# Kernel optimization log

Hardware: AMD Instinct MI355X
Metric: run time of the kernel (lower is better)

## Reference

```python
import jax, jax.numpy as jnp
import numpy as np

B, L, DM, H, DH = 2, 2048, 1024, 4, 128
TOT = H * DH  # 512


def _dwconv(x, w, b, L):
    # x: (B,L,C), w: (C,1,4) depthwise, padding=3 then causal trim to L (matches Conv1d(padding=3)[...,:L])
    y = jax.lax.conv_general_dilated(x.transpose(0, 2, 1), w, (1,), [(3, 3)],
                                     dimension_numbers=('NCH', 'OIH', 'NCH'),
                                     feature_group_count=w.shape[0])
    y = y[..., :L] + b[None, :, None]
    return y.transpose(0, 2, 1)


def _l2norm(x):
    return x / jnp.maximum(jnp.linalg.norm(x, axis=-1, keepdims=True), 1e-12)


def setup_inputs() -> dict:
    key = jax.random.key(0)
    ks = jax.random.split(key, 16)
    s = 0.02
    return {
        'x': jax.random.normal(ks[0], (B, L, DM), jnp.float32),
        'state': jnp.zeros((B, H, DH, DH), jnp.float32),
        'Wq': jax.random.normal(ks[1], (TOT, DM), jnp.float32) * s,
        'Wk': jax.random.normal(ks[2], (TOT, DM), jnp.float32) * s,
        'Wv': jax.random.normal(ks[3], (2 * TOT, DM), jnp.float32) * s,
        'Wa': jax.random.normal(ks[4], (H, DM), jnp.float32) * s,
        'Wb': jax.random.normal(ks[5], (H, DM), jnp.float32) * s,
        'Wg': jax.random.normal(ks[6], (TOT, DM), jnp.float32) * s,
        'Wo': jax.random.normal(ks[7], (DM, TOT), jnp.float32) * s,
        'qcw': jax.random.normal(ks[8], (TOT, 1, 4), jnp.float32) * 0.1,
        'qcb': jnp.zeros((TOT,), jnp.float32),
        'kcw': jax.random.normal(ks[9], (TOT, 1, 4), jnp.float32) * 0.1,
        'kcb': jnp.zeros((TOT,), jnp.float32),
        'vcw': jax.random.normal(ks[10], (2 * TOT, 1, 4), jnp.float32) * 0.1,
        'vcb': jnp.zeros((2 * TOT,), jnp.float32),
        'ln_w': jnp.ones((TOT,), jnp.float32),
        'ln_b': jnp.zeros((TOT,), jnp.float32),
    }


def reference(x, state, Wq, Wk, Wv, Wa, Wb, Wg, Wo, qcw, qcb, kcw, kcb, vcw, vcb, ln_w, ln_b):
    Bn, Ln, _ = x.shape
    q = _dwconv(x @ Wq.T, qcw, qcb, Ln)
    k = _dwconv(x @ Wk.T, kcw, kcb, Ln)
    v = _dwconv(x @ Wv.T, vcw, vcb, Ln)
    # silu then L2-normalize over the FULL total_dim (before head split), as in the source
    q = _l2norm(jax.nn.silu(q))
    k = _l2norm(jax.nn.silu(k))
    v = jax.nn.silu(v)
    alpha = jax.nn.sigmoid(x @ Wa.T)  # (B,L,H)
    beta = jax.nn.sigmoid(x @ Wb.T)   # (B,L,H)
    q = q.reshape(Bn, Ln, H, DH)
    k = k.reshape(Bn, Ln, H, DH)
    v_main, v_gate = jnp.split(v, 2, axis=-1)
    v_main = v_main.reshape(Bn, Ln, H, DH)
    v_gate = v_gate.reshape(Bn, Ln, H, DH)

    def step(S, inp):
        q_t, k_t, v_t, a_t, b_t = inp  # (B,H,D),(B,H,D),(B,H,D),(B,H),(B,H)
        a = a_t[..., None, None]
        b = b_t[..., None, None]
        Sk = jnp.einsum('bhij,bhj->bhi', S, k_t)  # S @ k
        # S @ (alpha*(I - beta k k^T)) + beta v k^T, via rank-1 update
        S = a * (S - b * (Sk[..., :, None] * k_t[..., None, :])) \
            + b * (v_t[..., :, None] * k_t[..., None, :])
        o = jnp.einsum('bhij,bhj->bhi', S, q_t)
        return S, o

    xs = (q.transpose(1, 0, 2, 3), k.transpose(1, 0, 2, 3), v_main.transpose(1, 0, 2, 3),
          alpha.transpose(1, 0, 2), beta.transpose(1, 0, 2))
    final_state, outs = jax.lax.scan(step, state, xs)
    out = outs.transpose(1, 0, 2, 3)  # (B,L,H,D)

    out = (out * v_gate).reshape(Bn, Ln, TOT)
    out = out * jax.nn.silu(x @ Wg.T)
    mu = out.mean(-1, keepdims=True)
    var = jnp.mean((out - mu) ** 2, axis=-1, keepdims=True)
    out = (out - mu) * jax.lax.rsqrt(var + 1e-5) * ln_w + ln_b
    out = out @ Wo.T
    return out, final_state
```

## Files before the change

kernel.cpp:

```cpp
#include <hip/hip_runtime.h>
#include <hip/hip_bf16.h>

#define BQ    2
#define LQ    2048
#define DMQ   1024
#define HQ    4
#define DHQ   128
#define TOTQ  512
#define BLQ   4096
#define NPROJ 2688
#define KPROJ 1024
#define CT    64
#define NCH   32

typedef short bf16x8 __attribute__((ext_vector_type(8)));
typedef short s16x4  __attribute__((ext_vector_type(4)));
typedef float f32x4  __attribute__((ext_vector_type(4)));

#define MFMA16(a, b, c) __builtin_amdgcn_mfma_f32_16x16x32_bf16(a, b, c, 0, 0, 0)

__device__ __forceinline__ float siluf(float x) { return x / (1.f + __expf(-x)); }
__device__ __forceinline__ float sigf(float x)  { return 1.f / (1.f + __expf(-x)); }
__device__ __forceinline__ short bf16s(float x) {
  return __builtin_bit_cast(short, __float2bfloat16(x));
}
__device__ __forceinline__ float bfu2f(unsigned short u) {
  return __bfloat162float(__builtin_bit_cast(__hip_bfloat16, u));
}
__device__ __forceinline__ bf16x8 pack8(f32x4 a, f32x4 b) {
  bf16x8 r;
  r[0] = bf16s(a.x); r[1] = bf16s(a.y); r[2] = bf16s(a.z); r[3] = bf16s(a.w);
  r[4] = bf16s(b.x); r[5] = bf16s(b.y); r[6] = bf16s(b.z); r[7] = bf16s(b.w);
  return r;
}

__device__ __forceinline__ void gload_lds16(const void* g, void* l) {
  __builtin_amdgcn_global_load_lds(
      (__attribute__((address_space(1))) void*)(unsigned long long)g,
      (__attribute__((address_space(3))) void*)(unsigned int)(unsigned long long)l,
      16, 0, 0);
}

__global__ __launch_bounds__(256)
void cast_f32_bf16_kernel(const float* __restrict__ src, __hip_bfloat16* __restrict__ dst, int n4)
{
  int i = blockIdx.x * 256 + threadIdx.x;
  if (i < n4) {
    float4 v = ((const float4*)src)[i];
    __hip_bfloat16 o[4] = { __float2bfloat16(v.x), __float2bfloat16(v.y),
                            __float2bfloat16(v.z), __float2bfloat16(v.w) };
    *(ushort4*)((unsigned short*)dst + (size_t)i * 4) = *(ushort4*)o;
  }
}

__global__ __launch_bounds__(256)
void cast_wcat_kernel(const float* __restrict__ Wq, const float* __restrict__ Wk,
                      const float* __restrict__ Wv, const float* __restrict__ Wg,
                      const float* __restrict__ Wa, const float* __restrict__ Wb,
                      __hip_bfloat16* __restrict__ Wcat)
{
  int i4 = blockIdx.x * 256 + threadIdx.x;
  int row = i4 >> 8;
  int col = (i4 & 255) * 4;
  int idx = row * 1024 + col;
  float4 v;
  if      (row < 512)  v = *(const float4*)(Wq + idx);
  else if (row < 1024) v = *(const float4*)(Wk + idx - 512 * 1024);
  else if (row < 2048) v = *(const float4*)(Wv + idx - 1024 * 1024);
  else if (row < 2560) v = *(const float4*)(Wg + idx - 2048 * 1024);
  else if (row < 2564) v = *(const float4*)(Wa + (row - 2560) * 1024 + col);
  else if (row < 2568) v = *(const float4*)(Wb + (row - 2564) * 1024 + col);
  else                 v = make_float4(0.f, 0.f, 0.f, 0.f);
  __hip_bfloat16 o[4] = { __float2bfloat16(v.x), __float2bfloat16(v.y),
                          __float2bfloat16(v.z), __float2bfloat16(v.w) };
  *(ushort4*)((unsigned short*)Wcat + idx) = *(ushort4*)o;
}

template <typename TOUT>
__global__ __launch_bounds__(256)
void gemm_bt_kernel(const __hip_bfloat16* __restrict__ A,
                    const __hip_bfloat16* __restrict__ Bw,
                    TOUT* __restrict__ C, int M, int N, int K,
                    float* __restrict__ aux, int auxc0)
{
  __shared__ __hip_bfloat16 As[2 * 128 * 32];
  __shared__ __hip_bfloat16 Bs[2 * 128 * 32];
  const int tid  = threadIdx.x;
  const int lane = tid & 63;
  const int w    = tid >> 6;
  const int wm   = w >> 1, wn = w & 1;
  const int tm   = blockIdx.x, tn = blockIdx.y;
  const int lr   = lane & 15, lk = lane >> 4;

  f32x4 acc[4][4] = {};

  const int e0   = tid * 8;
  const int srow = e0 >> 5;
  const int scol = e0 & 31;
  const __hip_bfloat16* Ap = A  + (size_t)(tm * 128 + srow) * K + scol;
  const __hip_bfloat16* Bp = Bw + (size_t)(tn * 128 + srow) * K + scol;
  char* AsB  = (char*)As;
  char* BsB  = (char*)Bs;
  const size_t half = (size_t)64 * K;
  const int nk = K >> 5;

  {
    char* AsD = AsB + w * 1024;
    char* BsD = BsB + w * 1024;
    gload_lds16(Ap,        AsD);
    gload_lds16(Ap + half, AsD + 4096);
    gload_lds16(Bp,        BsD);
    gload_lds16(Bp + half, BsD + 4096);
  }
  __syncthreads();

  for (int it = 0; it < nk; ++it) {
    const int sel = it & 1;
    if (it + 1 < nk) {
      const int kk = (it + 1) * 32;
      char* AsD = AsB + ((sel ^ 1) * 8192) + w * 1024;
      char* BsD = BsB + ((sel ^ 1) * 8192) + w * 1024;
      gload_lds16(Ap + kk,        AsD);
      gload_lds16(Ap + half + kk, AsD + 4096);
      gload_lds16(Bp + kk,        BsD);
      gload_lds16(Bp + half + kk, BsD + 4096);
    }
    const char* AsR = AsB + sel * 8192;
    const char* BsR = BsB + sel * 8192;
    bf16x8 af[4], bfv[4];
#pragma unroll
    for (int m = 0; m < 4; ++m)
      af[m]  = *(const bf16x8*)(AsR + ((wm * 64 + m * 16 + lr) * 32 + lk * 8) * 2);
#pragma unroll
    for (int n = 0; n < 4; ++n)
      bfv[n] = *(const bf16x8*)(BsR + ((wn * 64 + n * 16 + lr) * 32 + lk * 8) * 2);
#pragma unroll
    for (int m = 0; m < 4; ++m)
#pragma unroll
      for (int n = 0; n < 4; ++n)
        acc[m][n] = MFMA16(af[m], bfv[n], acc[m][n]);
    __syncthreads();
  }

  const int crow0 = tm * 128 + wm * 64 + (lane >> 4) * 4;
  const int ccol0 = tn * 128 + wn * 64 + lr;
#pragma unroll
  for (int m = 0; m < 4; ++m)
#pragma unroll
    for (int n = 0; n < 4; ++n) {
      const int cc = ccol0 + n * 16;
#pragma unroll
      for (int j = 0; j < 4; ++j) {
        const float v = acc[m][n][j];
        const size_t row = (size_t)(crow0 + m * 16 + j);
        if constexpr (sizeof(TOUT) == 2)
          ((unsigned short*)C)[row * N + cc] = (unsigned short)bf16s(v);
        else
          C[row * N + cc] = v;
        if (aux && cc >= auxc0 && cc < auxc0 + 8)
          aux[row * 8 + (cc - auxc0)] = v;
      }
    }
}

__global__ __launch_bounds__(256)
void conv_act_kernel(const __hip_bfloat16* __restrict__ C, const float* __restrict__ abf,
                     const float* __restrict__ qcw, const float* __restrict__ qcb,
                     const float* __restrict__ kcw, const float* __restrict__ kcb,
                     const float* __restrict__ vcw, const float* __restrict__ vcb,
                     __hip_bfloat16* __restrict__ qh, __hip_bfloat16* __restrict__ kh,
                     __hip_bfloat16* __restrict__ vm, __hip_bfloat16* __restrict__ vg,
                     float* __restrict__ al, float* __restrict__ be)
{
  const int blk = blockIdx.x;
  const int bl0 = blk * 8;
  const int t0  = bl0 & (LQ - 1);
  const int tid = threadIdx.x;
  const unsigned short* Cu = (const unsigned short*)C;
  __shared__ float red[4][16];

  float2 qv[8], kv[8];
  float sq[8], sk[8];
#pragma unroll
  for (int t = 0; t < 8; ++t) { sq[t] = 0.f; sk[t] = 0.f; }

  {
    const int c0 = tid * 2;
    const float4 wqA = *(const float4*)(qcw + 4 * c0);
    const float4 wqB = *(const float4*)(qcw + 4 * c0 + 4);
    const float4 wkA = *(const float4*)(kcw + 4 * c0);
    const float4 wkB = *(const float4*)(kcw + 4 * c0 + 4);
    const float2 bq = *(const float2*)(qcb + c0);
    const float2 bk = *(const float2*)(kcb + c0);
    float2 wrq[11], wrk[11];
#pragma unroll
    for (int r = 0; r < 11; ++r) {
      const int tt = t0 - 3 + r;
      if (tt >= 0) {
        const unsigned short* Cr = Cu + (size_t)(bl0 - 3 + r) * NPROJ;
        const ushort2 aq = *(const ushort2*)(Cr + c0);
        const ushort2 ak = *(const ushort2*)(Cr + 512 + c0);
        wrq[r] = make_float2(bfu2f(aq.x), bfu2f(aq.y));
        wrk[r] = make_float2(bfu2f(ak.x), bfu2f(ak.y));
      } else {
        wrq[r] = make_float2(0.f, 0.f);
        wrk[r] = make_float2(0.f, 0.f);
      }
    }
#pragma unroll
    for (int t = 0; t < 8; ++t) {
      float aq0 = bq.x, aq1 = bq.y, ak0 = bk.x, ak1 = bk.y;
#pragma unroll
      for (int j = 0; j < 4; ++j) {
        aq0 = fmaf(((const float*)&wqA)[j], wrq[t + j].x, aq0);
        aq1 = fmaf(((const float*)&wqB)[j], wrq[t + j].y, aq1);
        ak0 = fmaf(((const float*)&wkA)[j], wrk[t + j].x, ak0);
        ak1 = fmaf(((const float*)&wkB)[j], wrk[t + j].y, ak1);
      }
      const float q0 = siluf(aq0), q1 = siluf(aq1);
      const float k0 = siluf(ak0), k1 = siluf(ak1);
      qv[t] = make_float2(q0, q1);
      kv[t] = make_float2(k0, k1);
      sq[t] = fmaf(q1, q1, fmaf(q0, q0, sq[t]));
      sk[t] = fmaf(k1, k1, fmaf(k0, k0, sk[t]));
    }
  }
#pragma unroll
  for (int m = 1; m < 64; m <<= 1) {
#pragma unroll
    for (int t = 0; t < 8; ++t) {
      sq[t] += __shfl_xor(sq[t], m);
      sk[t] += __shfl_xor(sk[t], m);
    }
  }
  {
    const int w = tid >> 6, lane = tid & 63;
    if (lane == 0) {
#pragma unroll
      for (int t = 0; t < 8; ++t) { red[w][t] = sq[t]; red[w][8 + t] = sk[t]; }
    }
  }
  __syncthreads();
  float rnq[8], rnk[8];
#pragma unroll
  for (int t = 0; t < 8; ++t) {
    const float SQ = red[0][t] + red[1][t] + red[2][t] + red[3][t];
    const float SK = red[0][8 + t] + red[1][8 + t] + red[2][8 + t] + red[3][8 + t];
    rnq[t] = 1.f / fmaxf(sqrtf(SQ), 1e-12f);
    rnk[t] = 1.f / fmaxf(sqrtf(SK), 1e-12f);
  }
  {
    const int c0 = tid * 2;
#pragma unroll
    for (int t = 0; t < 8; ++t) {
      ushort2 oq, ok;
      oq.x = (unsigned short)bf16s(qv[t].x * rnq[t]);
      oq.y = (unsigned short)bf16s(qv[t].y * rnq[t]);
      ok.x = (unsigned short)bf16s(kv[t].x * rnk[t]);
      ok.y = (unsigned short)bf16s(kv[t].y * rnk[t]);
      *(ushort2*)((unsigned short*)qh + (size_t)(bl0 + t) * 512 + c0) = oq;
      *(ushort2*)((unsigned short*)kh + (size_t)(bl0 + t) * 512 + c0) = ok;
    }
  }
  {
    const int cv = tid * 4;
    const float4 wv0 = *(const float4*)(vcw + 4 * cv);
    const float4 wv1 = *(const float4*)(vcw + 4 * cv + 4);
    const float4 wv2 = *(const float4*)(vcw + 4 * cv + 8);
    const float4 wv3 = *(const float4*)(vcw + 4 * cv + 12);
    const float4 bv4 = *(const float4*)(vcb + cv);
    float4 wr[11];
#pragma unroll
    for (int r = 0; r < 11; ++r) {
      const int tt = t0 - 3 + r;
      if (tt >= 0) {
        const ushort4 u = *(const ushort4*)(Cu + (size_t)(bl0 - 3 + r) * NPROJ + 1024 + cv);
        wr[r] = make_float4(bfu2f(u.x), bfu2f(u.y), bfu2f(u.z), bfu2f(u.w));
      } else {
        wr[r] = make_float4(0.f, 0.f, 0.f, 0.f);
      }
    }
#pragma unroll
    for (int t = 0; t < 8; ++t) {
      float a0 = bv4.x, a1 = bv4.y, a2 = bv4.z, a3 = bv4.w;
#pragma unroll
      for (int j = 0; j < 4; ++j) {
        a0 = fmaf(((const float*)&wv0)[j], ((const float*)&wr[t + j])[0], a0);
        a1 = fmaf(((const float*)&wv1)[j], ((const float*)&wr[t + j])[1], a1);
        a2 = fmaf(((const float*)&wv2)[j], ((const float*)&wr[t + j])[2], a2);
        a3 = fmaf(((const float*)&wv3)[j], ((const float*)&wr[t + j])[3], a3);
      }
      ushort4 o;
      o.x = (unsigned short)bf16s(siluf(a0));
      o.y = (unsigned short)bf16s(siluf(a1));
      o.z = (unsigned short)bf16s(siluf(a2));
      o.w = (unsigned short)bf16s(siluf(a3));
      if (cv < 512) *(ushort4*)((unsigned short*)vm + (size_t)(bl0 + t) * 512 + cv)         = o;
      else          *(ushort4*)((unsigned short*)vg + (size_t)(bl0 + t) * 512 + (cv - 512)) = o;
    }
  }
  if (tid < 64) {
    const int t = tid >> 3;
    const int k = tid & 7;
    const float v = abf[(size_t)(bl0 + t) * 8 + k];
    if (k < 4) al[(size_t)(bl0 + t) * 4 + k]       = sigf(v);
    else       be[(size_t)(bl0 + t) * 4 + (k - 4)] = sigf(v);
  }
}

__global__ __launch_bounds__(256)
void scan_phaseA_kernel(const __hip_bfloat16* __restrict__ qh, const __hip_bfloat16* __restrict__ kh,
                        const __hip_bfloat16* __restrict__ vm, const float* __restrict__ al,
                        const float* __restrict__ be,
                        short* __restrict__ WTB, short* __restrict__ ZB,
                        short* __restrict__ PHB, float* __restrict__ GV,
                        short* __restrict__ TRB, float* __restrict__ BF)
{
  __shared__ char sm[136192];
  float* Xl = (float*)(sm);
  __hip_bfloat16* KBl = (__hip_bfloat16*)(sm);
  __hip_bfloat16* QBl = (__hip_bfloat16*)(sm + 17408);
  float* Ll  = (float*)(sm + 65536);
  float* dv  = (float*)(sm + 82944);
  float* bv  = (float*)(sm + 83200);
  float* gbv = (float*)(sm + 83456);
  float* fvs = (float*)(sm + 83712);
  short* KTl  = (short*)(sm + 83968);
  short* WTFl = (short*)(sm + 101376);
  short* ZFl  = (short*)(sm + 118784);

  const int cb = blockIdx.x;
  const int bh = cb & 7, c = cb >> 3;
  const int b = bh >> 2, h = bh & 3;
  const int tid = threadIdx.x;
  const int lane = tid & 63;
  const int w = tid >> 6;
  const int lr = lane & 15, lk = lane >> 4;
  const size_t rowbase = (size_t)(b * LQ + c * CT) * 512 + h * 128;

#pragma unroll
  for (int rep = 0; rep < 4; ++rep) {
    const int fid = tid + rep * 256;
    const int r = fid >> 4;
    const int cg = (fid & 15) * 8;
    *(bf16x8*)(KBl + r * 136 + cg) = *(const bf16x8*)(kh + rowbase + (size_t)r * 512 + cg);
    *(bf16x8*)(QBl + r * 136 + cg) = *(const bf16x8*)(qh + rowbase + (size_t)r * 512 + cg);
  }
  if (w == 0) {
    float la = __logf(al[(size_t)(b * LQ + c * CT + lane) * 4 + h]);
    const float bb = be[(size_t)(b * LQ + c * CT + lane) * 4 + h];
#pragma unroll
    for (int off = 1; off < 64; off <<= 1) {
      const float tv = __shfl_up(la, off, 64);
      if (lane >= off) la += tv;
    }
    dv[lane] = la; bv[lane] = bb; gbv[lane] = bb * __expf(la);
    const float d63 = __shfl(la, 63, 64);
    fvs[lane] = __expf(d63 - la);
    GV[cb * 64 + lane] = __expf(la);
  }
  __syncthreads();

  f32x4 aG[4] = {}, aP[4] = {};
#pragma unroll
  for (int ks = 0; ks < 4; ++ks) {
    bf16x8 bk[4];
#pragma unroll
    for (int nt = 0; nt < 4; ++nt)
      bk[nt] = *(const bf16x8*)(KBl + (nt * 16 + lr) * 136 + ks * 32 + lk * 8);
    const bf16x8 ak = *(const bf16x8*)(KBl + (w * 16 + lr) * 136 + ks * 32 + lk * 8);
    const bf16x8 aq = *(const bf16x8*)(QBl + (w * 16 + lr) * 136 + ks * 32 + lk * 8);
#pragma unroll
    for (int nt = 0; nt < 4; ++nt) {
      aG[nt] = MFMA16(ak, bk[nt], aG[nt]);
      aP[nt] = MFMA16(aq, bk[nt], aP[nt]);
    }
  }
#pragma unroll
  for (int nt = 0; nt < 4; ++nt)
#pragma unroll
    for (int jj = 0; jj < 4; ++jj) {
      const int t = w * 16 + lk * 4 + jj;
      const int s = nt * 16 + lr;
      const float eg = __expf(dv[t] - dv[s]);
      Ll[t * 68 + s] = (t > s) ? bv[t] * eg * aG[nt][jj] : 0.f;
      PHB[(size_t)cb * 4096 + t * 64 + s] = (s <= t) ? bf16s(eg * aP[nt][jj]) : (short)0;
    }
  if (tid < 128) {
    const short* Kbs = (const short*)KBl;
#pragma unroll
    for (int s4 = 0; s4 < 16; ++s4) {
      s16x4 pk;
#pragma unroll
      for (int e = 0; e < 4; ++e)
        pk[e] = Kbs[(s4 * 4 + e) * 136 + tid];
      *(s16x4*)(KTl + tid * 68 + s4 * 4) = pk;
    }
  }
  __syncthreads();

  const int j = tid;
  const __hip_bfloat16* src = (j < 128) ? kh : vm;
  const __hip_bfloat16* xp = src + rowbase + (j & 127);
  float* XlC = Xl + j;
  short* dstN = (j < 128) ? (WTB + (size_t)cb * 8192 + j)
                          : (ZB  + (size_t)cb * 8192 + (j - 128));
  short* dstT = (j < 128) ? (WTFl + j * 68)
                          : (ZFl  + (j - 128) * 68);

  for (int r = 0; r < 4; ++r) {
    float u[16];
#pragma unroll
    for (int i = 0; i < 16; ++i) {
      const int t = r * 16 + i;
      u[i] = __bfloat162float(xp[(size_t)t * 512]) * ((j < 128) ? gbv[t] : bv[t]);
    }
    for (int sc = 0; sc < r; ++sc) {
      float xs[16];
#pragma unroll
      for (int k = 0; k < 16; ++k) xs[k] = XlC[(sc * 16 + k) * 256];
#pragma unroll
      for (int i = 0; i < 16; ++i) {
        const float* lrow = Ll + (r * 16 + i) * 68 + sc * 16;
        const f32x4 l0 = *(const f32x4*)(lrow);
        const f32x4 l1 = *(const f32x4*)(lrow + 4);
        const f32x4 l2 = *(const f32x4*)(lrow + 8);
        const f32x4 l3 = *(const f32x4*)(lrow + 12);
        f32x4 acc = {};
        acc.x = fmaf(l0.x, xs[0],  acc.x); acc.y = fmaf(l0.y, xs[1],  acc.y);
        acc.z = fmaf(l0.z, xs[2],  acc.z); acc.w = fmaf(l0.w, xs[3],  acc.w);
        acc.x = fmaf(l1.x, xs[4],  acc.x); acc.y = fmaf(l1.y, xs[5],  acc.y);
        acc.z = fmaf(l1.z, xs[6],  acc.z); acc.w = fmaf(l1.w, xs[7],  acc.w);
        acc.x = fmaf(l2.x, xs[8],  acc.x); acc.y = fmaf(l2.y, xs[9],  acc.y);
        acc.z = fmaf(l2.z, xs[10], acc.z); acc.w = fmaf(l2.w, xs[11], acc.w);
        acc.x = fmaf(l3.x, xs[12], acc.x); acc.y = fmaf(l3.y, xs[13], acc.y);
        acc.z = fmaf(l3.z, xs[14], acc.z); acc.w = fmaf(l3.w, xs[15], acc.w);
        u[i] -= (acc.x + acc.y) + (acc.z + acc.w);
      }
    }
#pragma unroll
    for (int i = 1; i < 16; ++i) {
      const float* lrow = Ll + (r * 16 + i) * 68 + r * 16;
      f32x4 acc = {};
#pragma unroll
      for (int k4 = 0; k4 < 4; ++k4) {
        if (k4 * 4 < i) {
          const f32x4 lv = *(const f32x4*)(lrow + k4 * 4);
          acc.x = fmaf(lv.x, u[k4 * 4 + 0], acc.x);
          acc.y = fmaf(lv.y, u[k4 * 4 + 1], acc.y);
          acc.z = fmaf(lv.z, u[k4 * 4 + 2], acc.z);
          acc.w = fmaf(lv.w, u[k4 * 4 + 3], acc.w);
        }
      }
      u[i] -= (acc.x + acc.y) + (acc.z + acc.w);
    }
    if (r < 3) {
#pragma unroll
      for (int i = 0; i < 16; ++i) XlC[(r * 16 + i) * 256] = u[i];
    }
#pragma unroll
    for (int i = 0; i < 16; ++i)
      dstN[(r * 16 + i) * 128] = bf16s(u[i]);
#pragma unroll
    for (int s4 = 0; s4 < 4; ++s4) {
      s16x4 p;
#pragma unroll
      for (int e = 0; e < 4; ++e)
        p[e] = bf16s(fvs[r * 16 + s4 * 4 + e] * u[s4 * 4 + e]);
      *(s16x4*)(dstT + r * 16 + s4 * 4) = p;
    }
  }
  __syncthreads();

  const float gc = __expf(dv[63]);
  {
    f32x4 acc[2][8] = {};
#pragma unroll
    for (int ks = 0; ks < 2; ++ks) {
      const bf16x8 a0 = *(const bf16x8*)(KTl + (w * 32 + lr) * 68 + ks * 32 + lk * 8);
      const bf16x8 a1 = *(const bf16x8*)(KTl + (w * 32 + 16 + lr) * 68 + ks * 32 + lk * 8);
#pragma unroll
      for (int nt = 0; nt < 8; ++nt) {
        const bf16x8 bm = *(const bf16x8*)(WTFl + (nt * 16 + lr) * 68 + ks * 32 + lk * 8);
        acc[0][nt] = MFMA16(a0, bm, acc[0][nt]);
        acc[1][nt] = MFMA16(a1, bm, acc[1][nt]);
      }
    }
#pragma unroll
    for (int mt = 0; mt < 2; ++mt)
#pragma unroll
      for (int nt = 0; nt < 8; ++nt)
#pragma unroll
        for (int jj = 0; jj < 4; ++jj) {
          const int jr = w * 32 + mt * 16 + lk * 4 + jj;
          const int m  = nt * 16 + lr;
          const float v = ((jr == m) ? gc : 0.f) - acc[mt][nt][jj];
          TRB[(size_t)cb * 16384 + jr * 128 + m] = bf16s(v);
        }
  }
  {
    f32x4 acc[2][8] = {};
#pragma unroll
    for (int ks = 0; ks < 2; ++ks) {
      const bf16x8 a0 = *(const bf16x8*)(ZFl + (w * 32 + lr) * 68 + ks * 32 + lk * 8);
      const bf16x8 a1 = *(const bf16x8*)(ZFl + (w * 32 + 16 + lr) * 68 + ks * 32 + lk * 8);
#pragma unroll
      for (int nt = 0; nt < 8; ++nt) {
        const bf16x8 bj = *(const bf16x8*)(KTl + (nt * 16 + lr) * 68 + ks * 32 + lk * 8);
        acc[0][nt] = MFMA16(a0, bj, acc[0][nt]);
        acc[1][nt] = MFMA16(a1, bj, acc[1][nt]);
      }
    }
#pragma unroll
    for (int mt = 0; mt < 2; ++mt)
#pragma unroll
      for (int nt = 0; nt < 8; ++nt)
#pragma unroll
        for (int jj = 0; jj < 4; ++jj) {
          const int ir = w * 32 + mt * 16 + lk * 4 + jj;
          const int jc = nt * 16 + lr;
          BF[(size_t)cb * 16384 + ir * 128 + jc] = acc[mt][nt][jj];
        }
  }
}

#define L2_PREFETCH(BT, BA, CC) do {                                               \
  const int cbn_ = (CC) * 8 + bh;                                                  \
  _Pragma("unroll") for (int nt = 0; nt < 2; ++nt) {                               \
    _Pragma("unroll") for (int ks = 0; ks < 4; ++ks)                               \
      BT[nt][ks] = *(const bf16x8*)(TRB + (size_t)cbn_ * 16384 +                   \
                                    (w * 32 + nt * 16 + lr) * 128 + ks * 32 + lk * 8); \
    _Pragma("unroll") for (int jj = 0; jj < 4; ++jj)                               \
      BA[nt][jj] = BF[(size_t)cbn_ * 16384 + (r0 + lk * 4 + jj) * 128 +            \
                      w * 32 + nt * 16 + lr];                                      \
  }                                                                                \
} while (0)

#define L2_STEP(BT, BA, CC, PBT, PBA) do {                                         \
  const int cb_ = (CC) * 8 + bh;                                                   \
  { const int idx = tid * 8, r = idx >> 7, jc = idx & 127;                         \
    f32x4 s0 = *(const f32x4*)&Scur[r * 132 + jc];                                 \
    f32x4 s1 = *(const f32x4*)&Scur[r * 132 + jc + 4];                             \
    *(bf16x8*)(SALL + (size_t)cb_ * 16384 + (r0 + r) * 128 + jc) = pack8(s0, s1); }\
  bf16x8 af[4];                                                                    \
  _Pragma("unroll") for (int ks = 0; ks < 4; ++ks)                                 \
    af[ks] = pack8(*(const f32x4*)&Scur[lr * 132 + ks * 32 + lk * 8],              \
                   *(const f32x4*)&Scur[lr * 132 + ks * 32 + lk * 8 + 4]);         \
  if ((CC) < 31) L2_PREFETCH(PBT, PBA, (CC) + 1);                                  \
  f32x4 acc0 = {}, acc1 = {};                                                      \
  _Pragma("unroll") for (int ks = 0; ks < 4; ++ks) {                               \
    acc0 = MFMA16(af[ks], BT[0][ks], acc0);                                        \
    acc1 = MFMA16(af[ks], BT[1][ks], acc1);                                        \
  }                                                                                \
  _Pragma("unroll") for (int jj = 0; jj < 4; ++jj) {                               \
    Snxt[(lk * 4 + jj) * 132 + w * 32 + lr]      = acc0[jj] + BA[0][jj];           \
    Snxt[(lk * 4 + jj) * 132 + w * 32 + 16 + lr] = acc1[jj] + BA[1][jj];           \
  }                                                                                \
  __syncthreads();                                                                 \
  { float* t_ = Scur; Scur = Snxt; Snxt = t_; }                                    \
} while (0)

__global__ __launch_bounds__(256)
void scan_state_kernel(const short* __restrict__ TRB, const float* __restrict__ BF,
                       const float* __restrict__ st0, short* __restrict__ SALL,
                       float* __restrict__ stout)
{
  __shared__ float Sl[2 * 16 * 132];
  const int bid = blockIdx.x;
  const int bh = bid & 7, slab = bid >> 3;
  const int r0 = slab * 16;
  const int tid = threadIdx.x, lane = tid & 63, w = tid >> 6;
  const int lr = lane & 15, lk = lane >> 4;

  float* Scur = Sl;
  float* Snxt = Sl + 16 * 132;

  {
    const int idx = tid * 8, r = idx >> 7, jc = idx & 127;
    const float* sp = st0 + ((size_t)bh * 128 + r0 + r) * 128 + jc;
    *(f32x4*)&Scur[r * 132 + jc]     = *(const f32x4*)sp;
    *(f32x4*)&Scur[r * 132 + jc + 4] = *(const f32x4*)(sp + 4);
  }
  bf16x8 btA[2][4], btB[2][4];
  float  baA[2][4], baB[2][4];
  L2_PREFETCH(btA, baA, 0);
  __syncthreads();

  for (int c2 = 0; c2 < 16; ++c2) {
    L2_STEP(btA, baA, 2 * c2,     btB, baB);
    L2_STEP(btB, baB, 2 * c2 + 1, btA, baA);
  }

  {
    const int idx = tid * 8, r = idx >> 7, jc = idx & 127;
    float* sp = stout + ((size_t)bh * 128 + r0 + r) * 128 + jc;
    *(f32x4*)sp       = *(const f32x4*)&Scur[r * 132 + jc];
    *(f32x4*)(sp + 4) = *(const f32x4*)&Scur[r * 132 + jc + 4];
  }
}

__global__ __launch_bounds__(512)
void scan_output_kernel(const __hip_bfloat16* __restrict__ qh,
                        const short* __restrict__ WTB, const __hip_bfloat16* __restrict__ ZB,
                        const short* __restrict__ PHB, const float* __restrict__ GV,
                        const short* __restrict__ SALL, float* __restrict__ obuf)
{
  __shared__ short Ut[128 * 72];
  const int cb = blockIdx.x;
  const int bh = cb & 7, c = cb >> 3;
  const int b = bh >> 2, h = bh & 3;
  const int tid = threadIdx.x, lane = tid & 63, w = tid >> 6;
  const int lr = lane & 15, lk = lane >> 4;
  const int r0 = (w & 3) * 16;

  f32x4 Y[8] = {};
#pragma unroll
  for (int ks = 0; ks < 4; ++ks) {
    bf16x8 af;
    if (w < 4) {
      af = *(const bf16x8*)(qh + ((size_t)(b * LQ + c * CT) + r0 + lr) * 512 + h * 128 + ks * 32 + lk * 8);
    } else {
      af = *(const bf16x8*)(WTB + (size_t)cb * 8192 + (r0 + lr) * 128 + ks * 32 + lk * 8);
    }
#pragma unroll
    for (int nt = 0; nt < 8; ++nt) {
      const bf16x8 bs = *(const bf16x8*)(SALL + (size_t)cb * 16384 + (nt * 16 + lr) * 128 + ks * 32 + lk * 8);
      Y[nt] = MFMA16(af, bs, Y[nt]);
    }
  }
  if (w >= 4) {
#pragma unroll
    for (int nt = 0; nt < 8; ++nt) {
      const int i = nt * 16 + lr;
      s16x4 up;
#pragma unroll
      for (int jj = 0; jj < 4; ++jj) {
        const int s = r0 + lk * 4 + jj;
        const float z = __bfloat162float(ZB[(size_t)cb * 8192 + s * 128 + i]);
        up[jj] = bf16s(z - Y[nt][jj]);
      }
      *(s16x4*)&Ut[i * 72 + r0 + lk * 4] = up;
    }
  }
  __syncthreads();
  if (w < 4) {
    f32x4 P2[8] = {};
#pragma unroll
    for (int ks = 0; ks < 2; ++ks) {
      const bf16x8 ap = *(const bf16x8*)(PHB + (size_t)cb * 4096 + (r0 + lr) * 64 + ks * 32 + lk * 8);
#pragma unroll
      for (int nt = 0; nt < 8; ++nt) {
        const bf16x8 bu = *(const bf16x8*)&Ut[(nt * 16 + lr) * 72 + ks * 32 + lk * 8];
        P2[nt] = MFMA16(ap, bu, P2[nt]);
      }
    }
    float gvv[4];
#pragma unroll
    for (int jj = 0; jj < 4; ++jj) gvv[jj] = GV[cb * 64 + r0 + lk * 4 + jj];
#pragma unroll
    for (int nt = 0; nt < 8; ++nt) {
      const int i = nt * 16 + lr;
#pragma unroll
      for (int jj = 0; jj < 4; ++jj) {
        const int t = r0 + lk * 4 + jj;
        obuf[((size_t)(b * LQ + c * CT) + t) * 512 + h * 128 + i] =
            gvv[jj] * Y[nt][jj] + P2[nt][jj];
      }
    }
  }
}

__global__ __launch_bounds__(256)
void gate_ln_kernel(const float* __restrict__ obuf, const __hip_bfloat16* __restrict__ vg,
                    const __hip_bfloat16* __restrict__ C, const float* __restrict__ lnw,
                    const float* __restrict__ lnb, __hip_bfloat16* __restrict__ lno)
{
  const int bl = blockIdx.x, tid = threadIdx.x;
  const int c0 = tid * 2;
  __shared__ float red[8];
  const float2 ov = *(const float2*)(obuf + (size_t)bl * 512 + c0);
  const ushort2 gvu = *(const ushort2*)((const unsigned short*)vg + (size_t)bl * 512 + c0);
  const ushort2 ggu = *(const ushort2*)((const unsigned short*)C + (size_t)bl * NPROJ + 2048 + c0);
  const float v0 = ov.x * bfu2f(gvu.x) * siluf(bfu2f(ggu.x));
  const float v1 = ov.y * bfu2f(gvu.y) * siluf(bfu2f(ggu.y));
  float s = v0 + v1;
  float s2 = fmaf(v1, v1, v0 * v0);
  float2 pr = make_float2(s, s2);
#pragma unroll
  for (int m = 1; m < 64; m <<= 1) { pr.x += __shfl_xor(pr.x, m); pr.y += __shfl_xor(pr.y, m); }
  if ((tid & 63) == 0) { red[(tid >> 6) * 2] = pr.x; red[(tid >> 6) * 2 + 1] = pr.y; }
  __syncthreads();
  const float S  = red[0] + red[2] + red[4] + red[6];
  const float S2 = red[1] + red[3] + red[5] + red[7];
  const float mu  = S * (1.f / 512.f);
  const float var = S2 * (1.f / 512.f) - mu * mu;
  const float rs  = rsqrtf(var + 1e-5f);
  const float2 lw = *(const float2*)(lnw + c0);
  const float2 lb = *(const float2*)(lnb + c0);
  __hip_bfloat16 o[2] = {
    __float2bfloat16(fmaf((v0 - mu) * rs, lw.x, lb.x)),
    __float2bfloat16(fmaf((v1 - mu) * rs, lw.y, lb.y)) };
  *(ushort2*)((unsigned short*)lno + (size_t)bl * 512 + c0) = *(ushort2*)o;
}

extern "C" void kernel_launch(void* const* d_in, const int* in_sizes, int n_in,
                              void* d_out, int out_size, void* d_ws, size_t ws_size,
                              hipStream_t stream)
{
  (void)in_sizes; (void)n_in; (void)out_size; (void)ws_size;
  const float* x    = (const float*)d_in[0];
  const float* st0  = (const float*)d_in[1];
  const float* Wq   = (const float*)d_in[2];
  const float* Wk   = (const float*)d_in[3];
  const float* Wv   = (const float*)d_in[4];
  const float* Wa   = (const float*)d_in[5];
  const float* Wb   = (const float*)d_in[6];
  const float* Wg   = (const float*)d_in[7];
  const float* Wo   = (const float*)d_in[8];
  const float* qcw  = (const float*)d_in[9];
  const float* qcb  = (const float*)d_in[10];
  const float* kcw  = (const float*)d_in[11];
  const float* kcb  = (const float*)d_in[12];
  const float* vcw  = (const float*)d_in[13];
  const float* vcb  = (const float*)d_in[14];
  const float* lnw  = (const float*)d_in[15];
  const float* lnb  = (const float*)d_in[16];
  float* out = (float*)d_out;

  char* ws = (char*)d_ws;
  __hip_bfloat16* XB   = (__hip_bfloat16*)(ws + 0);
  __hip_bfloat16* LNO  = (__hip_bfloat16*)(ws + 0);
  short*          WTB  = (short*)(ws + 4194304);
  __hip_bfloat16* WCAT = (__hip_bfloat16*)(ws + 8388608);
  __hip_bfloat16* WOB  = (__hip_bfloat16*)(ws + 13893632);
  __hip_bfloat16* CBUFH = (__hip_bfloat16*)(ws + 14942208);
  __hip_bfloat16* QH   = (__hip_bfloat16*)(ws + 58982400);
  __hip_bfloat16* KH   = (__hip_bfloat16*)(ws + 67371008);
  __hip_bfloat16* VM   = (__hip_bfloat16*)(ws + 75759616);
  __hip_bfloat16* VG   = (__hip_bfloat16*)(ws + 84148224);
  float* AL   = (float*)(ws + 92536832);
  float* BE   = (float*)(ws + 92602368);
  float* OBUF = (float*)(ws + 92667904);
  short* TRB  = (short*)(ws + 92667904);
  short* PHB  = (short*)(ws + 105250816);
  short* ZB   = (short*)(ws + 107347968);
  float* GV   = (float*)(ws + 111542272);
  short* SALL = (short*)(ws + 115868672);
  float* ABF  = (float*)(ws + 124257280);
  float* BF   = (float*)(ws + 124388352);

  cast_f32_bf16_kernel<<<4096, 256, 0, stream>>>(x,  XB,  1048576);
  cast_f32_bf16_kernel<<<512,  256, 0, stream>>>(Wo, WOB, 131072);
  cast_wcat_kernel<<<2688, 256, 0, stream>>>(Wq, Wk, Wv, Wg, Wa, Wb, WCAT);

  gemm_bt_kernel<__hip_bfloat16><<<dim3(32, 21), 256, 0, stream>>>(
      XB, WCAT, CBUFH, BLQ, NPROJ, KPROJ, ABF, 2560);

  conv_act_kernel<<<512, 256, 0, stream>>>(CBUFH, ABF, qcw, qcb, kcw, kcb, vcw, vcb,
                                           QH, KH, VM, VG, AL, BE);

  scan_phaseA_kernel<<<256, 256, 0, stream>>>(QH, KH, VM, AL, BE,
                                              WTB, ZB, PHB, GV, TRB, BF);

  scan_state_kernel<<<64, 256, 0, stream>>>(TRB, BF, st0, SALL, out + 4194304);

  scan_output_kernel<<<256, 512, 0, stream>>>(QH, WTB, (const __hip_bfloat16*)ZB,
                                              PHB, GV, SALL, OBUF);

  gate_ln_kernel<<<BLQ, 256, 0, stream>>>(OBUF, VG, CBUFH, lnw, lnb, LNO);

  gemm_bt_kernel<float><<<dim3(32, 8), 256, 0, stream>>>(
      LNO, WOB, out, BLQ, DMQ, TOTQ, nullptr, 0);
}
```

Measured before the change: 151.4 us.

## Merge cast kernels, double phaseA threads, store scan output as bf16

Three cast kernels are fused into one launch to cut launch overhead. The scan phase-A kernel moves to 512 threads: MFMA tiles are split across 8 waves and the triangular forward-substitution is split into two halves with extra barriers. The scan output buffer is stored as bf16 instead of fp32, halving traffic into the gate/layernorm kernel at some precision cost. The added syncthreads in the substitution loop and the halved per-thread work may limit the gain.

```diff
diff --git a/kernel.cpp b/kernel.cpp
--- a/kernel.cpp
+++ b/kernel.cpp
@@ -42,38 +42,44 @@
 }
 
 __global__ __launch_bounds__(256)
-void cast_f32_bf16_kernel(const float* __restrict__ src, __hip_bfloat16* __restrict__ dst, int n4)
+void cast_all_kernel(const float* __restrict__ x, const float* __restrict__ Wo,
+                     const float* __restrict__ Wq, const float* __restrict__ Wk,
+                     const float* __restrict__ Wv, const float* __restrict__ Wg,
+                     const float* __restrict__ Wa, const float* __restrict__ Wb,
+                     __hip_bfloat16* __restrict__ XB, __hip_bfloat16* __restrict__ WOB,
+                     __hip_bfloat16* __restrict__ Wcat)
 {
-  int i = blockIdx.x * 256 + threadIdx.x;
-  if (i < n4) {
-    float4 v = ((const float4*)src)[i];
+  const int bid = blockIdx.x;
+  const int tid = threadIdx.x;
+  if (bid < 4096) {
+    const int i = bid * 256 + tid;
+    float4 v = ((const float4*)x)[i];
     __hip_bfloat16 o[4] = { __float2bfloat16(v.x), __float2bfloat16(v.y),
                             __float2bfloat16(v.z), __float2bfloat16(v.w) };
-    *(ushort4*)((unsigned short*)dst + (size_t)i * 4) = *(ushort4*)o;
-  }
-}
-
-__global__ __launch_bounds__(256)
-void cast_wcat_kernel(const float* __restrict__ Wq, const float* __restrict__ Wk,
-                      const float* __restrict__ Wv, const float* __restrict__ Wg,
-                      const float* __restrict__ Wa, const float* __restrict__ Wb,
-                      __hip_bfloat16* __restrict__ Wcat)
-{
-  int i4 = blockIdx.x * 256 + threadIdx.x;
-  int row = i4 >> 8;
-  int col = (i4 & 255) * 4;
-  int idx = row * 1024 + col;
-  float4 v;
-  if      (row < 512)  v = *(const float4*)(Wq + idx);
-  else if (row < 1024) v = *(const float4*)(Wk + idx - 512 * 1024);
-  else if (row < 2048) v = *(const float4*)(Wv + idx - 1024 * 1024);
-  else if (row < 2560) v = *(const float4*)(Wg + idx - 2048 * 1024);
-  else if (row < 2564) v = *(const float4*)(Wa + (row - 2560) * 1024 + col);
-  else if (row < 2568) v = *(const float4*)(Wb + (row - 2564) * 1024 + col);
-  else                 v = make_float4(0.f, 0.f, 0.f, 0.f);
-  __hip_bfloat16 o[4] = { __float2bfloat16(v.x), __float2bfloat16(v.y),
-                          __float2bfloat16(v.z), __float2bfloat16(v.w) };
-  *(ushort4*)((unsigned short*)Wcat + idx) = *(ushort4*)o;
+    *(ushort4*)((unsigned short*)XB + (size_t)i * 4) = *(ushort4*)o;
+  } else if (bid < 4608) {
+    const int i = (bid - 4096) * 256 + tid;
+    float4 v = ((const float4*)Wo)[i];
+    __hip_bfloat16 o[4] = { __float2bfloat16(v.x), __float2bfloat16(v.y),
+                            __float2bfloat16(v.z), __float2bfloat16(v.w) };
+    *(ushort4*)((unsigned short*)WOB + (size_t)i * 4) = *(ushort4*)o;
+  } else {
+    const int i4 = (bid - 4608) * 256 + tid;
+    const int row = i4 >> 8;
+    const int col = (i4 & 255) * 4;
+    const int idx = row * 1024 + col;
+    float4 v;
+    if      (row < 512)  v = *(const float4*)(Wq + idx);
+    else if (row < 1024) v = *(const float4*)(Wk + idx - 512 * 1024);
+    else if (row < 2048) v = *(const float4*)(Wv + idx - 1024 * 1024);
+    else if (row < 2560) v = *(const float4*)(Wg + idx - 2048 * 1024);
+    else if (row < 2564) v = *(const float4*)(Wa + (row - 2560) * 1024 + col);
+    else if (row < 2568) v = *(const float4*)(Wb + (row - 2564) * 1024 + col);
+    else                 v = make_float4(0.f, 0.f, 0.f, 0.f);
+    __hip_bfloat16 o[4] = { __float2bfloat16(v.x), __float2bfloat16(v.y),
+                            __float2bfloat16(v.z), __float2bfloat16(v.w) };
+    *(ushort4*)((unsigned short*)Wcat + idx) = *(ushort4*)o;
+  }
 }
 
 template <typename TOUT>
@@ -308,7 +314,7 @@
   }
 }
 
-__global__ __launch_bounds__(256)
+__global__ __launch_bounds__(512)
 void scan_phaseA_kernel(const __hip_bfloat16* __restrict__ qh, const __hip_bfloat16* __restrict__ kh,
                         const __hip_bfloat16* __restrict__ vm, const float* __restrict__ al,
                         const float* __restrict__ be,
@@ -339,8 +345,8 @@
   const size_t rowbase = (size_t)(b * LQ + c * CT) * 512 + h * 128;
 
 #pragma unroll
-  for (int rep = 0; rep < 4; ++rep) {
-    const int fid = tid + rep * 256;
+  for (int rep = 0; rep < 2; ++rep) {
+    const int fid = tid + rep * 512;
     const int r = fid >> 4;
     const int cg = (fid & 15) * 8;
     *(bf16x8*)(KBl + r * 136 + cg) = *(const bf16x8*)(kh + rowbase + (size_t)r * 512 + cg);
@@ -361,31 +367,35 @@
   }
   __syncthreads();
 
-  f32x4 aG[4] = {}, aP[4] = {};
-#pragma unroll
-  for (int ks = 0; ks < 4; ++ks) {
-    bf16x8 bk[4];
-#pragma unroll
-    for (int nt = 0; nt < 4; ++nt)
-      bk[nt] = *(const bf16x8*)(KBl + (nt * 16 + lr) * 136 + ks * 32 + lk * 8);
-    const bf16x8 ak = *(const bf16x8*)(KBl + (w * 16 + lr) * 136 + ks * 32 + lk * 8);
-    const bf16x8 aq = *(const bf16x8*)(QBl + (w * 16 + lr) * 136 + ks * 32 + lk * 8);
-#pragma unroll
-    for (int nt = 0; nt < 4; ++nt) {
-      aG[nt] = MFMA16(ak, bk[nt], aG[nt]);
-      aP[nt] = MFMA16(aq, bk[nt], aP[nt]);
-    }
-  }
-#pragma unroll
-  for (int nt = 0; nt < 4; ++nt)
-#pragma unroll
-    for (int jj = 0; jj < 4; ++jj) {
-      const int t = w * 16 + lk * 4 + jj;
-      const int s = nt * 16 + lr;
-      const float eg = __expf(dv[t] - dv[s]);
-      Ll[t * 68 + s] = (t > s) ? bv[t] * eg * aG[nt][jj] : 0.f;
-      PHB[(size_t)cb * 4096 + t * 64 + s] = (s <= t) ? bf16s(eg * aP[nt][jj]) : (short)0;
-    }
+  {
+    const int tb = (w & 3) * 16;
+    const int sh = (w >> 2) * 2;
+    f32x4 aG[2] = {}, aP[2] = {};
+#pragma unroll
+    for (int ks = 0; ks < 4; ++ks) {
+      bf16x8 bk[2];
+#pragma unroll
+      for (int nt = 0; nt < 2; ++nt)
+        bk[nt] = *(const bf16x8*)(KBl + ((sh + nt) * 16 + lr) * 136 + ks * 32 + lk * 8);
+      const bf16x8 ak = *(const bf16x8*)(KBl + (tb + lr) * 136 + ks * 32 + lk * 8);
+      const bf16x8 aq = *(const bf16x8*)(QBl + (tb + lr) * 136 + ks * 32 + lk * 8);
+#pragma unroll
+      for (int nt = 0; nt < 2; ++nt) {
+        aG[nt] = MFMA16(ak, bk[nt], aG[nt]);
+        aP[nt] = MFMA16(aq, bk[nt], aP[nt]);
+      }
+    }
+#pragma unroll
+    for (int nt = 0; nt < 2; ++nt)
+#pragma unroll
+      for (int jj = 0; jj < 4; ++jj) {
+        const int t = tb + lk * 4 + jj;
+        const int s = (sh + nt) * 16 + lr;
+        const float eg = __expf(dv[t] - dv[s]);
+        Ll[t * 68 + s] = (t > s) ? bv[t] * eg * aG[nt][jj] : 0.f;
+        PHB[(size_t)cb * 4096 + t * 64 + s] = (s <= t) ? bf16s(eg * aP[nt][jj]) : (short)0;
+      }
+  }
   if (tid < 128) {
     const short* Kbs = (const short*)KBl;
 #pragma unroll
@@ -399,7 +409,9 @@
   }
   __syncthreads();
 
-  const int j = tid;
+  const int j = tid & 255;
+  const int half = tid >> 8;
+  const int i0 = half * 8;
   const __hip_bfloat16* src = (j < 128) ? kh : vm;
   const __hip_bfloat16* xp = src + rowbase + (j & 127);
   float* XlC = Xl + j;
@@ -409,10 +421,10 @@
                           : (ZFl  + (j - 128) * 68);
 
   for (int r = 0; r < 4; ++r) {
-    float u[16];
-#pragma unroll
-    for (int i = 0; i < 16; ++i) {
-      const int t = r * 16 + i;
+    float u[8];
+#pragma unroll
+    for (int i = 0; i < 8; ++i) {
+      const int t = r * 16 + i0 + i;
       u[i] = __bfloat162float(xp[(size_t)t * 512]) * ((j < 128) ? gbv[t] : bv[t]);
     }
     for (int sc = 0; sc < r; ++sc) {
@@ -420,8 +432,8 @@
 #pragma unroll
       for (int k = 0; k < 16; ++k) xs[k] = XlC[(sc * 16 + k) * 256];
 #pragma unroll
-      for (int i = 0; i < 16; ++i) {
-        const float* lrow = Ll + (r * 16 + i) * 68 + sc * 16;
+      for (int i = 0; i < 8; ++i) {
+        const float* lrow = Ll + (r * 16 + i0 + i) * 68 + sc * 16;
         const f32x4 l0 = *(const f32x4*)(lrow);
         const f32x4 l1 = *(const f32x4*)(lrow + 4);
         const f32x4 l2 = *(const f32x4*)(lrow + 8);
@@ -438,50 +450,97 @@
         u[i] -= (acc.x + acc.y) + (acc.z + acc.w);
       }
     }
-#pragma unroll
-    for (int i = 1; i < 16; ++i) {
-      const float* lrow = Ll + (r * 16 + i) * 68 + r * 16;
-      f32x4 acc = {};
-#pragma unroll
-      for (int k4 = 0; k4 < 4; ++k4) {
-        if (k4 * 4 < i) {
-          const f32x4 lv = *(const f32x4*)(lrow + k4 * 4);
-          acc.x = fmaf(lv.x, u[k4 * 4 + 0], acc.x);
-          acc.y = fmaf(lv.y, u[k4 * 4 + 1], acc.y);
-          acc.z = fmaf(lv.z, u[k4 * 4 + 2], acc.z);
-          acc.w = fmaf(lv.w, u[k4 * 4 + 3], acc.w);
+    if (half == 0) {
+#pragma unroll
+      for (int i = 1; i < 8; ++i) {
+        const float* lrow = Ll + (r * 16 + i) * 68 + r * 16;
+        f32x4 acc = {};
+#pragma unroll
+        for (int k4 = 0; k4 < 2; ++k4) {
+          if (k4 * 4 < i) {
+            const f32x4 lv = *(const f32x4*)(lrow + k4 * 4);
+            acc.x = fmaf(lv.x, u[k4 * 4 + 0], acc.x);
+            acc.y = fmaf(lv.y, u[k4 * 4 + 1], acc.y);
+            acc.z = fmaf(lv.z, u[k4 * 4 + 2], acc.z);
+            acc.w = fmaf(lv.w, u[k4 * 4 + 3], acc.w);
+          }
         }
-      }
-      u[i] -= (acc.x + acc.y) + (acc.z + acc.w);
-    }
-    if (r < 3) {
-#pragma unroll
-      for (int i = 0; i < 16; ++i) XlC[(r * 16 + i) * 256] = u[i];
-    }
-#pragma unroll
-    for (int i = 0; i < 16; ++i)
-      dstN[(r * 16 + i) * 128] = bf16s(u[i]);
-#pragma unroll
-    for (int s4 = 0; s4 < 4; ++s4) {
-      s16x4 p;
-#pragma unroll
-      for (int e = 0; e < 4; ++e)
-        p[e] = bf16s(fvs[r * 16 + s4 * 4 + e] * u[s4 * 4 + e]);
-      *(s16x4*)(dstT + r * 16 + s4 * 4) = p;
-    }
-  }
-  __syncthreads();
+        u[i] -= (acc.x + acc.y) + (acc.z + acc.w);
+      }
+#pragma unroll
+      for (int i = 0; i < 8; ++i) XlC[(r * 16 + i) * 256] = u[i];
+#pragma unroll
+      for (int i = 0; i < 8; ++i) dstN[(r * 16 + i) * 128] = bf16s(u[i]);
+#pragma unroll
+      for (int s4 = 0; s4 < 2; ++s4) {
+        s16x4 p;
+#pragma unroll
+        for (int e = 0; e < 4; ++e)
+          p[e] = bf16s(fvs[r * 16 + s4 * 4 + e] * u[s4 * 4 + e]);
+        *(s16x4*)(dstT + r * 16 + s4 * 4) = p;
+      }
+    }
+    __syncthreads();
+    if (half == 1) {
+      float xa[8];
+#pragma unroll
+      for (int k = 0; k < 8; ++k) xa[k] = XlC[(r * 16 + k) * 256];
+#pragma unroll
+      for (int i = 0; i < 8; ++i) {
+        const float* lrow = Ll + (r * 16 + 8 + i) * 68 + r * 16;
+        const f32x4 l0 = *(const f32x4*)(lrow);
+        const f32x4 l1 = *(const f32x4*)(lrow + 4);
+        f32x4 acc = {};
+        acc.x = fmaf(l0.x, xa[0], acc.x); acc.y = fmaf(l0.y, xa[1], acc.y);
+        acc.z = fmaf(l0.z, xa[2], acc.z); acc.w = fmaf(l0.w, xa[3], acc.w);
+        acc.x = fmaf(l1.x, xa[4], acc.x); acc.y = fmaf(l1.y, xa[5], acc.y);
+        acc.z = fmaf(l1.z, xa[6], acc.z); acc.w = fmaf(l1.w, xa[7], acc.w);
+        u[i] -= (acc.x + acc.y) + (acc.z + acc.w);
+      }
+#pragma unroll
+      for (int i = 1; i < 8; ++i) {
+        const float* lrow = Ll + (r * 16 + 8 + i) * 68 + r * 16 + 8;
+        f32x4 acc = {};
+#pragma unroll
+        for (int k4 = 0; k4 < 2; ++k4) {
+          if (k4 * 4 < i) {
+            const f32x4 lv = *(const f32x4*)(lrow + k4 * 4);
+            acc.x = fmaf(lv.x, u[k4 * 4 + 0], acc.x);
+            acc.y = fmaf(lv.y, u[k4 * 4 + 1], acc.y);
+            acc.z = fmaf(lv.z, u[k4 * 4 + 2], acc.z);
+            acc.w = fmaf(lv.w, u[k4 * 4 + 3], acc.w);
+          }
+        }
+        u[i] -= (acc.x + acc.y) + (acc.z + acc.w);
+      }
+#pragma unroll
+      for (int i = 0; i < 8; ++i) XlC[(r * 16 + 8 + i) * 256] = u[i];
+#pragma unroll
+      for (int i = 0; i < 8; ++i) dstN[(r * 16 + 8 + i) * 128] = bf16s(u[i]);
+#pragma unroll
+      for (int s4 = 0; s4 < 2; ++s4) {
+        s16x4 p;
+#pragma unroll
+        for (int e = 0; e < 4; ++e)
+          p[e] = bf16s(fvs[r * 16 + 8 + s4 * 4 + e] * u[s4 * 4 + e]);
+        *(s16x4*)(dstT + r * 16 + 8 + s4 * 4) = p;
+      }
+    }
+    __syncthreads();
+  }
 
   const float gc = __expf(dv[63]);
-  {
-    f32x4 acc[2][8] = {};
+  const int rb = (w & 3) * 32;
+  const int cq = (w >> 2) * 4;
+  {
+    f32x4 acc[2][4] = {};
 #pragma unroll
     for (int ks = 0; ks < 2; ++ks) {
-      const bf16x8 a0 = *(const bf16x8*)(KTl + (w * 32 + lr) * 68 + ks * 32 + lk * 8);
-      const bf16x8 a1 = *(const bf16x8*)(KTl + (w * 32 + 16 + lr) * 68 + ks * 32 + lk * 8);
-#pragma unroll
-      for (int nt = 0; nt < 8; ++nt) {
-        const bf16x8 bm = *(const bf16x8*)(WTFl + (nt * 16 + lr) * 68 + ks * 32 + lk * 8);
+      const bf16x8 a0 = *(const bf16x8*)(KTl + (rb + lr) * 68 + ks * 32 + lk * 8);
+      const bf16x8 a1 = *(const bf16x8*)(KTl + (rb + 16 + lr) * 68 + ks * 32 + lk * 8);
+#pragma unroll
+      for (int nt = 0; nt < 4; ++nt) {
+        const bf16x8 bm = *(const bf16x8*)(WTFl + ((cq + nt) * 16 + lr) * 68 + ks * 32 + lk * 8);
         acc[0][nt] = MFMA16(a0, bm, acc[0][nt]);
         acc[1][nt] = MFMA16(a1, bm, acc[1][nt]);
       }
@@ -489,24 +548,24 @@
 #pragma unroll
     for (int mt = 0; mt < 2; ++mt)
 #pragma unroll
-      for (int nt = 0; nt < 8; ++nt)
+      for (int nt = 0; nt < 4; ++nt)
 #pragma unroll
         for (int jj = 0; jj < 4; ++jj) {
-          const int jr = w * 32 + mt * 16 + lk * 4 + jj;
-          const int m  = nt * 16 + lr;
+          const int jr = rb + mt * 16 + lk * 4 + jj;
+          const int m  = (cq + nt) * 16 + lr;
           const float v = ((jr == m) ? gc : 0.f) - acc[mt][nt][jj];
           TRB[(size_t)cb * 16384 + jr * 128 + m] = bf16s(v);
         }
   }
   {
-    f32x4 acc[2][8] = {};
+    f32x4 acc[2][4] = {};
 #pragma unroll
     for (int ks = 0; ks < 2; ++ks) {
-      const bf16x8 a0 = *(const bf16x8*)(ZFl + (w * 32 + lr) * 68 + ks * 32 + lk * 8);
-      const bf16x8 a1 = *(const bf16x8*)(ZFl + (w * 32 + 16 + lr) * 68 + ks * 32 + lk * 8);
-#pragma unroll
-      for (int nt = 0; nt < 8; ++nt) {
-        const bf16x8 bj = *(const bf16x8*)(KTl + (nt * 16 + lr) * 68 + ks * 32 + lk * 8);
+      const bf16x8 a0 = *(const bf16x8*)(ZFl + (rb + lr) * 68 + ks * 32 + lk * 8);
+      const bf16x8 a1 = *(const bf16x8*)(ZFl + (rb + 16 + lr) * 68 + ks * 32 + lk * 8);
+#pragma unroll
+      for (int nt = 0; nt < 4; ++nt) {
+        const bf16x8 bj = *(const bf16x8*)(KTl + ((cq + nt) * 16 + lr) * 68 + ks * 32 + lk * 8);
         acc[0][nt] = MFMA16(a0, bj, acc[0][nt]);
         acc[1][nt] = MFMA16(a1, bj, acc[1][nt]);
       }
@@ -514,11 +573,11 @@
 #pragma unroll
     for (int mt = 0; mt < 2; ++mt)
 #pragma unroll
-      for (int nt = 0; nt < 8; ++nt)
+      for (int nt = 0; nt < 4; ++nt)
 #pragma unroll
         for (int jj = 0; jj < 4; ++jj) {
-          const int ir = w * 32 + mt * 16 + lk * 4 + jj;
-          const int jc = nt * 16 + lr;
+          const int ir = rb + mt * 16 + lk * 4 + jj;
+          const int jc = (cq + nt) * 16 + lr;
           BF[(size_t)cb * 16384 + ir * 128 + jc] = acc[mt][nt][jj];
         }
   }
@@ -603,7 +662,7 @@
 void scan_output_kernel(const __hip_bfloat16* __restrict__ qh,
                         const short* __restrict__ WTB, const __hip_bfloat16* __restrict__ ZB,
                         const short* __restrict__ PHB, const float* __restrict__ GV,
-                        const short* __restrict__ SALL, float* __restrict__ obuf)
+                        const short* __restrict__ SALL, __hip_bfloat16* __restrict__ obuf)
 {
   __shared__ short Ut[128 * 72];
   const int cb = blockIdx.x;
@@ -663,26 +722,26 @@
 #pragma unroll
       for (int jj = 0; jj < 4; ++jj) {
         const int t = r0 + lk * 4 + jj;
-        obuf[((size_t)(b * LQ + c * CT) + t) * 512 + h * 128 + i] =
-            gvv[jj] * Y[nt][jj] + P2[nt][jj];
+        ((unsigned short*)obuf)[((size_t)(b * LQ + c * CT) + t) * 512 + h * 128 + i] =
+            (unsigned short)bf16s(gvv[jj] * Y[nt][jj] + P2[nt][jj]);
       }
     }
   }
 }
 
 __global__ __launch_bounds__(256)
-void gate_ln_kernel(const float* __restrict__ obuf, const __hip_bfloat16* __restrict__ vg,
+void gate_ln_kernel(const __hip_bfloat16* __restrict__ obuf, const __hip_bfloat16* __restrict__ vg,
                     const __hip_bfloat16* __restrict__ C, const float* __restrict__ lnw,
                     const float* __restrict__ lnb, __hip_bfloat16* __restrict__ lno)
 {
   const int bl = blockIdx.x, tid = threadIdx.x;
   const int c0 = tid * 2;
   __shared__ float red[8];
-  const float2 ov = *(const float2*)(obuf + (size_t)bl * 512 + c0);
+  const ushort2 ovu = *(const ushort2*)((const unsigned short*)obuf + (size_t)bl * 512 + c0);
   const ushort2 gvu = *(const ushort2*)((const unsigned short*)vg + (size_t)bl * 512 + c0);
   const ushort2 ggu = *(const ushort2*)((const unsigned short*)C + (size_t)bl * NPROJ + 2048 + c0);
-  const float v0 = ov.x * bfu2f(gvu.x) * siluf(bfu2f(ggu.x));
-  const float v1 = ov.y * bfu2f(gvu.y) * siluf(bfu2f(ggu.y));
+  const float v0 = bfu2f(ovu.x) * bfu2f(gvu.x) * siluf(bfu2f(ggu.x));
+  const float v1 = bfu2f(ovu.y) * bfu2f(gvu.y) * siluf(bfu2f(ggu.y));
   float s = v0 + v1;
   float s2 = fmaf(v1, v1, v0 * v0);
   float2 pr = make_float2(s, s2);
@@ -740,7 +799,7 @@
   __hip_bfloat16* VG   = (__hip_bfloat16*)(ws + 84148224);
   float* AL   = (float*)(ws + 92536832);
   float* BE   = (float*)(ws + 92602368);
-  float* OBUF = (float*)(ws + 92667904);
+  __hip_bfloat16* OBUF = (__hip_bfloat16*)(ws + 92667904);
   short* TRB  = (short*)(ws + 92667904);
   short* PHB  = (short*)(ws + 105250816);
   short* ZB   = (short*)(ws + 107347968);
@@ -749,9 +808,7 @@
   float* ABF  = (float*)(ws + 124257280);
   float* BF   = (float*)(ws + 124388352);
 
-  cast_f32_bf16_kernel<<<4096, 256, 0, stream>>>(x,  XB,  1048576);
-  cast_f32_bf16_kernel<<<512,  256, 0, stream>>>(Wo, WOB, 131072);
-  cast_wcat_kernel<<<2688, 256, 0, stream>>>(Wq, Wk, Wv, Wg, Wa, Wb, WCAT);
+  cast_all_kernel<<<7296, 256, 0, stream>>>(x, Wo, Wq, Wk, Wv, Wg, Wa, Wb, XB, WOB, WCAT);
 
   gemm_bt_kernel<__hip_bfloat16><<<dim3(32, 21), 256, 0, stream>>>(
       XB, WCAT, CBUFH, BLQ, NPROJ, KPROJ, ABF, 2560);
@@ -759,7 +816,7 @@
   conv_act_kernel<<<512, 256, 0, stream>>>(CBUFH, ABF, qcw, qcb, kcw, kcb, vcw, vcb,
                                            QH, KH, VM, VG, AL, BE);
 
-  scan_phaseA_kernel<<<256, 256, 0, stream>>>(QH, KH, VM, AL, BE,
+  scan_phaseA_kernel<<<256, 512, 0, stream>>>(QH, KH, VM, AL, BE,
                                               WTB, ZB, PHB, GV, TRB, BF);
 
   scan_state_kernel<<<64, 256, 0, stream>>>(TRB, BF, st0, SALL, out + 4194304);
```

Result: faster. 143.5 us, median of 2 (-5.2%).
